# Kernel tuning notes

Hardware: AMD Instinct MI355X
Metric: run time of the kernel (lower is better)

The kernel has to match this reference:

```python
import jax, jax.numpy as jnp
import numpy as np

N, F_IN, HID, H1, E = 50000, 512, 128, 4, 800000
NEG_SLOPE = 0.2

def setup_inputs() -> dict:
    key = jax.random.key(0)
    ks = jax.random.split(key, 10)
    s = lambda fan: 1.0 / np.sqrt(fan)
    x = jax.random.normal(ks[0], (N, F_IN), jnp.float32)
    edge_index = jax.random.randint(ks[1], (2, E), 0, N, jnp.int32)
    W1 = jax.random.normal(ks[2], (F_IN, H1 * HID), jnp.float32) * s(F_IN)
    a_src1 = jax.random.normal(ks[3], (H1, HID), jnp.float32) * s(HID)
    a_dst1 = jax.random.normal(ks[4], (H1, HID), jnp.float32) * s(HID)
    b1 = jnp.zeros((H1 * HID,), jnp.float32)
    W2 = jax.random.normal(ks[5], (H1 * HID, HID), jnp.float32) * s(H1 * HID)
    a_src2 = jax.random.normal(ks[6], (1, HID), jnp.float32) * s(HID)
    a_dst2 = jax.random.normal(ks[7], (1, HID), jnp.float32) * s(HID)
    b2 = jnp.zeros((HID,), jnp.float32)
    return {"x": x, "edge_index": edge_index, "W1": W1, "a_src1": a_src1,
            "a_dst1": a_dst1, "b1": b1, "W2": W2, "a_src2": a_src2,
            "a_dst2": a_dst2, "b2": b2}

def _gat(x, src, dst, W, a_src, a_dst, b, n):
    H, C = a_src.shape
    h = (x @ W).reshape(-1, H, C)                      # [N, H, C]
    # per-edge attention logits: alpha_src[src] + alpha_dst[dst]
    e = jax.nn.leaky_relu((h * a_src).sum(-1)[src] + (h * a_dst).sum(-1)[dst],
                          NEG_SLOPE)                   # [E', H]
    # segment softmax over destination node
    m = jax.ops.segment_max(e, dst, num_segments=n)
    p = jnp.exp(e - m[dst])
    denom = jax.ops.segment_sum(p, dst, num_segments=n)
    alpha = p / (denom[dst] + 1e-16)
    # weighted scatter-add aggregation
    out = jax.ops.segment_sum(h[src] * alpha[:, :, None], dst, num_segments=n)
    return out.reshape(-1, H * C) + b

def reference(x, edge_index, W1, a_src1, a_dst1, b1, W2, a_src2, a_dst2, b2):
    loops = jnp.arange(N, dtype=edge_index.dtype)      # add_self_loops=True
    src = jnp.concatenate([edge_index[0], loops])
    dst = jnp.concatenate([edge_index[1], loops])
    h = jax.nn.elu(_gat(x, src, dst, W1, a_src1, a_dst1, b1, N))
    return _gat(h, src, dst, W2, a_src2, a_dst2, b2, N)
```

## Files before the change

### kernel.cpp

```cpp
#include <hip/hip_runtime.h>
#include <hip/hip_bf16.h>
#include <math.h>

#define NEG_SLOPE 0.2f

constexpr int N_NODES = 50000;
constexpr int F_IN    = 512;
constexpr int HID     = 128;
constexpr int H1      = 4;
constexpr int E_EDGES = 800000;
constexpr int E_TOT   = E_EDGES + N_NODES;

typedef __attribute__((ext_vector_type(8))) short short8;
typedef __attribute__((ext_vector_type(4))) float floatx4;
typedef __attribute__((ext_vector_type(4))) unsigned short ushort4v;

__device__ __forceinline__ unsigned short f2bf(float f) {
  union { float f; unsigned int u; } v; v.f = f;
  unsigned int u = v.u + 0x7FFFu + ((v.u >> 16) & 1u);
  return (unsigned short)(u >> 16);
}
__device__ __forceinline__ float bf_lo(unsigned int u) {
  union { unsigned int u; float f; } v; v.u = u << 16; return v.f;
}
__device__ __forceinline__ float bf_hi(unsigned int u) {
  union { unsigned int u; float f; } v; v.u = u & 0xFFFF0000u; return v.f;
}

__device__ __forceinline__ void store_val(float* p, float v) { *p = v; }
__device__ __forceinline__ void store_val(unsigned short* p, float v) { *p = f2bf(v); }

template <int CPT>
__device__ __forceinline__ void store_vec(unsigned short* p, const float* v) {
#pragma unroll
  for (int c = 0; c < CPT; c += 4) {
    ushort4v o;
#pragma unroll
    for (int j = 0; j < 4; ++j) o[j] = f2bf(v[c + j]);
    *(ushort4v*)(p + c) = o;
  }
}
template <int CPT>
__device__ __forceinline__ void store_vec(float* p, const float* v) {
#pragma unroll
  for (int c = 0; c < CPT; c += 4) *(float4*)(p + c) = *(const float4*)(v + c);
}

__device__ __forceinline__ void async_load16(const void* g, void* lds) {
  __builtin_amdgcn_global_load_lds(
      (const __attribute__((address_space(1))) unsigned int*)g,
      (__attribute__((address_space(3))) unsigned int*)lds, 16, 0, 0);
}

__global__ void zero_int_kernel(int* p, int n) {
  int i = blockIdx.x * blockDim.x + threadIdx.x;
  if (i < n) p[i] = 0;
}

__global__ void hist_kernel(const int* __restrict__ ei, int* __restrict__ counts) {
  int i = blockIdx.x * blockDim.x + threadIdx.x;
  if (i < E_EDGES) {
    atomicAdd(&counts[ei[E_EDGES + i]], 1);
  } else if (i < E_TOT) {
    atomicAdd(&counts[i - E_EDGES], 1);
  }
}

__global__ void scan1_kernel(const int* __restrict__ cnt, int* __restrict__ part,
                             int* __restrict__ bsum, int n) {
  __shared__ int buf[256];
  int tid = threadIdx.x, i = blockIdx.x * 256 + tid;
  int v = (i < n) ? cnt[i] : 0;
  buf[tid] = v;
  __syncthreads();
  for (int s = 1; s < 256; s <<= 1) {
    int t = (tid >= s) ? buf[tid - s] : 0;
    __syncthreads();
    buf[tid] += t;
    __syncthreads();
  }
  if (i < n) part[i] = buf[tid] - v;
  if (tid == 255) bsum[blockIdx.x] = buf[255];
}

__global__ void scan2_kernel(int* __restrict__ bsum, int nb) {
  __shared__ int buf[256];
  int tid = threadIdx.x;
  int v = (tid < nb) ? bsum[tid] : 0;
  buf[tid] = v;
  __syncthreads();
  for (int s = 1; s < 256; s <<= 1) {
    int t = (tid >= s) ? buf[tid - s] : 0;
    __syncthreads();
    buf[tid] += t;
    __syncthreads();
  }
  if (tid < nb) bsum[tid] = buf[tid] - v;
  if (tid == 255) bsum[nb] = buf[255];
}

__global__ void scan3_kernel(const int* __restrict__ part, const int* __restrict__ bsum,
                             int* __restrict__ offs, int* __restrict__ cursor, int n) {
  int i = blockIdx.x * 256 + threadIdx.x;
  if (i < n) { offs[i] = part[i] + bsum[blockIdx.x]; cursor[i] = 0; }
  if (i == 0) offs[n] = bsum[(n + 255) / 256];
}

__global__ void scatter_kernel(const int* __restrict__ ei, const int* __restrict__ offs,
                               int* __restrict__ cursor, int* __restrict__ sorted_src) {
  int i = blockIdx.x * blockDim.x + threadIdx.x;
  if (i >= E_TOT) return;
  int s, d;
  if (i < E_EDGES) { s = ei[i]; d = ei[E_EDGES + i]; }
  else             { s = i - E_EDGES; d = s; }
  int pos = offs[d] + atomicAdd(&cursor[d], 1);
  sorted_src[pos] = s;
}

__global__ void tcast_kernel(const float* __restrict__ in, unsigned short* __restrict__ out,
                             int K, int N) {
  int idx = blockIdx.x * blockDim.x + threadIdx.x;
  if (idx >= K * N) return;
  int n = idx / K, k = idx - n * K;
  out[idx] = f2bf(in[k * N + n]);
}

template <bool CVT_A, typename OT>
__global__ __launch_bounds__(256) void gemm_bf16_kernel(
    const void* __restrict__ Araw, const unsigned short* __restrict__ Bt,
    OT* __restrict__ C, const float* __restrict__ a_srcp, const float* __restrict__ a_dstp,
    float* __restrict__ alpha_src, float* __restrict__ alpha_dst,
    int M, int N, int K, int Hn, int nRowTiles) {
  __shared__ unsigned short As[128 * 32];
  __shared__ unsigned short Bs[128 * 32];
  __shared__ float red_s[128][2];
  __shared__ float red_d[128][2];

  int grp = blockIdx.x / (8 * Hn);
  int w8 = blockIdx.x % (8 * Hn);
  int head = w8 >> 3;
  int rowTile = grp * 8 + (w8 & 7);
  if (rowTile >= nRowTiles) return;
  int row0 = rowTile * 128;
  int col0 = head * 128;

  int tid = threadIdx.x;
  int lane = tid & 63, wave = tid >> 6;
  int wm = wave & 1, wn = wave >> 1;
  int l15 = lane & 15, quad = lane >> 4;

  floatx4 acc[4][4];
#pragma unroll
  for (int i = 0; i < 4; ++i)
#pragma unroll
    for (int j = 0; j < 4; ++j) acc[i][j] = (floatx4){0.f, 0.f, 0.f, 0.f};

  int seg_b = wave * 2;
  int r_in = (lane >> 2);
  int c8 = (lane & 3) * 8;

  for (int k0 = 0; k0 < K; k0 += 32) {
#pragma unroll
    for (int p = 0; p < 2; ++p) {
      int seg = seg_b + p;
      int r = seg * 16 + r_in;
      int gc = col0 + r;
      async_load16(Bt + (size_t)gc * K + k0 + c8, &Bs[seg * 512]);
    }
    if constexpr (CVT_A) {
      const float* Af = (const float*)Araw;
#pragma unroll
      for (int p = 0; p < 4; ++p) {
        int lin = tid + p * 256;
        int r = lin >> 3;
        int q = lin & 7;
        int gr = row0 + r; if (gr >= M) gr = M - 1;
        float4 f = *(const float4*)(Af + (size_t)gr * K + k0 + q * 4);
        ushort4v o;
        o[0] = f2bf(f.x); o[1] = f2bf(f.y); o[2] = f2bf(f.z); o[3] = f2bf(f.w);
        *(ushort4v*)&As[r * 32 + q * 4] = o;
      }
    } else {
      const unsigned short* Ab = (const unsigned short*)Araw;
#pragma unroll
      for (int p = 0; p < 2; ++p) {
        int seg = seg_b + p;
        int r = seg * 16 + r_in;
        int gr = row0 + r; if (gr >= M) gr = M - 1;
        async_load16(Ab + (size_t)gr * K + k0 + c8, &As[seg * 512]);
      }
    }
    __syncthreads();

    short8 a[4], b[4];
#pragma unroll
    for (int mi = 0; mi < 4; ++mi)
      a[mi] = *(const short8*)&As[(wm * 64 + mi * 16 + l15) * 32 + quad * 8];
#pragma unroll
    for (int ni = 0; ni < 4; ++ni)
      b[ni] = *(const short8*)&Bs[(wn * 64 + ni * 16 + l15) * 32 + quad * 8];
#pragma unroll
    for (int mi = 0; mi < 4; ++mi)
#pragma unroll
      for (int ni = 0; ni < 4; ++ni)
        acc[mi][ni] = __builtin_amdgcn_mfma_f32_16x16x32_bf16(a[mi], b[ni], acc[mi][ni], 0, 0, 0);
    __syncthreads();
  }

  float a_s[4], a_d[4];
#pragma unroll
  for (int ni = 0; ni < 4; ++ni) {
    int cih = wn * 64 + ni * 16 + l15;
    a_s[ni] = a_srcp[head * HID + cih];
    a_d[ni] = a_dstp[head * HID + cih];
  }

#pragma unroll
  for (int mi = 0; mi < 4; ++mi) {
#pragma unroll
    for (int r = 0; r < 4; ++r) {
      int rloc = wm * 64 + mi * 16 + quad * 4 + r;
      int grow = row0 + rloc;
      float ps = 0.f, pd = 0.f;
#pragma unroll
      for (int ni = 0; ni < 4; ++ni) {
        float v = acc[mi][ni][r];
        ps += v * a_s[ni];
        pd += v * a_d[ni];
        if (grow < M) {
          int gcol = col0 + wn * 64 + ni * 16 + l15;
          store_val(&C[(size_t)grow * N + gcol], v);
        }
      }
#pragma unroll
      for (int off = 1; off < 16; off <<= 1) {
        ps += __shfl_xor(ps, off);
        pd += __shfl_xor(pd, off);
      }
      if (l15 == 0) { red_s[rloc][wn] = ps; red_d[rloc][wn] = pd; }
    }
  }
  __syncthreads();
  if (tid < 128) {
    int grow = row0 + tid;
    if (grow < M) {
      alpha_src[(size_t)grow * Hn + head] = red_s[tid][0] + red_s[tid][1];
      alpha_dst[(size_t)grow * Hn + head] = red_d[tid][0] + red_d[tid][1];
    }
  }
}

template <int H, typename OT>
__global__ __launch_bounds__(64) void aggregate_kernel(
    const unsigned short* __restrict__ h, const float* __restrict__ asrc,
    const float* __restrict__ adst, const int* __restrict__ offs,
    const int* __restrict__ sorted_src, const float* __restrict__ bias,
    OT* __restrict__ out, int apply_elu) {
  constexpr int CPT = 8;
  constexpr int CH = H * HID;
  constexpr int NCH = CH / CPT;
  constexpr int SLOTS = 64 / NCH;
  __shared__ float p_sh[64 * H];
  __shared__ int rowoff_sh[64];
  int node = blockIdx.x;
  int lane = threadIdx.x;
  int off = offs[node];
  int deg = offs[node + 1] - off;
  if (deg > 64) deg = 64;

  int s_i = 0;
  if (lane < deg) s_i = sorted_src[off + lane];
  rowoff_sh[lane] = s_i * CH;

  float ar[H];
#pragma unroll
  for (int hh = 0; hh < H; ++hh) ar[hh] = (lane < deg) ? asrc[s_i * H + hh] : 0.f;
#pragma unroll
  for (int hh = 0; hh < H; ++hh) {
    float v = ar[hh] + adst[node * H + hh];
    v = (v > 0.f) ? v : NEG_SLOPE * v;
    float lg = (lane < deg) ? v : -1e30f;
#pragma unroll
    for (int o = 32; o; o >>= 1) lg = fmaxf(lg, __shfl_xor(lg, o));
    float p = (lane < deg) ? expf(v - lg) : 0.f;
    float s = p;
#pragma unroll
    for (int o = 32; o; o >>= 1) s += __shfl_xor(s, o);
    p_sh[lane * H + hh] = p * (1.f / (s + 1e-16f));
  }
  __syncthreads();

  int chlane = lane % NCH;
  int slot = lane / NCH;
  int ch = chlane * CPT;
  int head = ch >> 7;

  float acc[CPT];
#pragma unroll
  for (int c = 0; c < CPT; ++c) acc[c] = 0.f;

  auto body = [&](int e) {
    float w = p_sh[e * H + head];
    uint4 u = *(const uint4*)(h + (size_t)(unsigned)rowoff_sh[e] + ch);
    acc[0] += bf_lo(u.x) * w;  acc[1] += bf_hi(u.x) * w;
    acc[2] += bf_lo(u.y) * w;  acc[3] += bf_hi(u.y) * w;
    acc[4] += bf_lo(u.z) * w;  acc[5] += bf_hi(u.z) * w;
    acc[6] += bf_lo(u.w) * w;  acc[7] += bf_hi(u.w) * w;
  };
  int e = slot;
  for (; e + 7 * SLOTS < deg; e += 8 * SLOTS) {
    body(e); body(e + SLOTS); body(e + 2 * SLOTS); body(e + 3 * SLOTS);
    body(e + 4 * SLOTS); body(e + 5 * SLOTS); body(e + 6 * SLOTS); body(e + 7 * SLOTS);
  }
  for (; e + SLOTS < deg; e += 2 * SLOTS) { body(e); body(e + SLOTS); }
  for (; e < deg; e += SLOTS) body(e);

#pragma unroll
  for (int o = NCH; o < 64; o <<= 1)
#pragma unroll
    for (int c = 0; c < CPT; ++c) acc[c] += __shfl_xor(acc[c], o);

  if (slot == 0) {
    float r[CPT];
#pragma unroll
    for (int c = 0; c < CPT; ++c) {
      float t = acc[c] + bias[ch + c];
      if (apply_elu) t = (t > 0.f) ? t : (expf(t) - 1.f);
      r[c] = t;
    }
    store_vec<CPT>(&out[(size_t)node * CH + ch], r);
  }
}

extern "C" void kernel_launch(void* const* d_in, const int* in_sizes, int n_in,
                              void* d_out, int out_size, void* d_ws, size_t ws_size,
                              hipStream_t stream) {
  const float* x      = (const float*)d_in[0];
  const int*   ei     = (const int*)d_in[1];
  const float* W1     = (const float*)d_in[2];
  const float* a_src1 = (const float*)d_in[3];
  const float* a_dst1 = (const float*)d_in[4];
  const float* b1     = (const float*)d_in[5];
  const float* W2     = (const float*)d_in[6];
  const float* a_src2 = (const float*)d_in[7];
  const float* a_dst2 = (const float*)d_in[8];
  const float* b2     = (const float*)d_in[9];
  float* out = (float*)d_out;

  float* ws   = (float*)d_ws;
  float* as1  = ws;
  float* ad1  = as1 + N_NODES * H1;
  float* as2  = ad1 + N_NODES * H1;
  float* ad2  = as2 + N_NODES;
  unsigned short* bufA = (unsigned short*)(ad2 + N_NODES);
  unsigned short* bufB = bufA + (size_t)N_NODES * 512;
  unsigned short* hmidb = bufA;
  unsigned short* h1b   = bufB;
  unsigned short* h2b   = bufB;
  unsigned short* W1t   = bufB + (size_t)N_NODES * 512;
  unsigned short* W2t   = W1t + 512 * 512;
  int* counts = (int*)(W2t + 128 * 512);
  int* cursor = counts + N_NODES;
  int* offs   = cursor + N_NODES;
  int* ssrc   = offs + N_NODES + 1;
  int* part   = ssrc + E_TOT;
  int* bsum   = part + N_NODES;

  constexpr int NB = (N_NODES + 255) / 256;
  constexpr int NRT = (N_NODES + 127) / 128;
  constexpr int NRT8 = ((NRT + 7) / 8) * 8;

  zero_int_kernel<<<(N_NODES + 255) / 256, 256, 0, stream>>>(counts, N_NODES);
  hist_kernel<<<(E_TOT + 255) / 256, 256, 0, stream>>>(ei, counts);
  scan1_kernel<<<NB, 256, 0, stream>>>(counts, part, bsum, N_NODES);
  scan2_kernel<<<1, 256, 0, stream>>>(bsum, NB);
  scan3_kernel<<<NB, 256, 0, stream>>>(part, bsum, offs, cursor, N_NODES);
  scatter_kernel<<<(E_TOT + 255) / 256, 256, 0, stream>>>(ei, offs, cursor, ssrc);

  tcast_kernel<<<(512 * 512 + 255) / 256, 256, 0, stream>>>(W1, W1t, 512, 512);
  tcast_kernel<<<(512 * 128 + 255) / 256, 256, 0, stream>>>(W2, W2t, 512, 128);

  gemm_bf16_kernel<true, unsigned short><<<NRT8 * H1, 256, 0, stream>>>(
      x, W1t, h1b, a_src1, a_dst1, as1, ad1, N_NODES, 512, 512, H1, NRT);
  aggregate_kernel<4, unsigned short><<<N_NODES, 64, 0, stream>>>(
      h1b, as1, ad1, offs, ssrc, b1, hmidb, 1);

  gemm_bf16_kernel<false, unsigned short><<<NRT8, 256, 0, stream>>>(
      hmidb, W2t, h2b, a_src2, a_dst2, as2, ad2, N_NODES, 128, 512, 1, NRT);
  aggregate_kernel<1, float><<<N_NODES, 64, 0, stream>>>(
      h2b, as2, ad2, offs, ssrc, b2, out, 0);
}
```

Baseline: 508.5 us.

## Split aggregation across two waves per block for both GAT layers

```diff
diff --git a/kernel.cpp b/kernel.cpp
--- a/kernel.cpp
+++ b/kernel.cpp
@@ -250,34 +250,37 @@
   }
 }
 
-template <int H, typename OT>
-__global__ __launch_bounds__(64) void aggregate_kernel(
+template <int H, int WPN, typename OT>
+__global__ __launch_bounds__(128) void aggregate_kernel(
     const unsigned short* __restrict__ h, const float* __restrict__ asrc,
     const float* __restrict__ adst, const int* __restrict__ offs,
     const int* __restrict__ sorted_src, const float* __restrict__ bias,
     OT* __restrict__ out, int apply_elu) {
   constexpr int CPT = 8;
   constexpr int CH = H * HID;
-  constexpr int NCH = CH / CPT;
+  constexpr int WCH = CH / WPN;
+  constexpr int NCH = WCH / CPT;
   constexpr int SLOTS = 64 / NCH;
-  __shared__ float p_sh[64 * H];
-  __shared__ int rowoff_sh[64];
-  int node = blockIdx.x;
-  int lane = threadIdx.x;
-  int off = offs[node];
-  int deg = offs[node + 1] - off;
+  __shared__ float p_sh[2][64 * H];
+  __shared__ int ro_sh[2][64];
+  int tid = threadIdx.x;
+  int lane = tid & 63, w = tid >> 6;
+  int node = (WPN == 2) ? blockIdx.x : blockIdx.x * 2 + w;
+  bool live = node < N_NODES;
+  int off = live ? offs[node] : 0;
+  int deg = live ? (offs[node + 1] - off) : 0;
   if (deg > 64) deg = 64;
 
   int s_i = 0;
   if (lane < deg) s_i = sorted_src[off + lane];
-  rowoff_sh[lane] = s_i * CH;
+  ro_sh[w][lane] = s_i * CH;
 
   float ar[H];
 #pragma unroll
   for (int hh = 0; hh < H; ++hh) ar[hh] = (lane < deg) ? asrc[s_i * H + hh] : 0.f;
 #pragma unroll
   for (int hh = 0; hh < H; ++hh) {
-    float v = ar[hh] + adst[node * H + hh];
+    float v = ar[hh] + (live ? adst[node * H + hh] : 0.f);
     v = (v > 0.f) ? v : NEG_SLOPE * v;
     float lg = (lane < deg) ? v : -1e30f;
 #pragma unroll
@@ -286,26 +289,28 @@
     float s = p;
 #pragma unroll
     for (int o = 32; o; o >>= 1) s += __shfl_xor(s, o);
-    p_sh[lane * H + hh] = p * (1.f / (s + 1e-16f));
+    p_sh[w][lane * H + hh] = p * (1.f / (s + 1e-16f));
   }
   __syncthreads();
 
   int chlane = lane % NCH;
   int slot = lane / NCH;
-  int ch = chlane * CPT;
+  int ch = (WPN == 2 ? w * WCH : 0) + chlane * CPT;
   int head = ch >> 7;
 
   float acc[CPT];
 #pragma unroll
   for (int c = 0; c < CPT; ++c) acc[c] = 0.f;
 
+  const float* pw = &p_sh[w][0];
+  const int* ro = &ro_sh[w][0];
   auto body = [&](int e) {
-    float w = p_sh[e * H + head];
-    uint4 u = *(const uint4*)(h + (size_t)(unsigned)rowoff_sh[e] + ch);
-    acc[0] += bf_lo(u.x) * w;  acc[1] += bf_hi(u.x) * w;
-    acc[2] += bf_lo(u.y) * w;  acc[3] += bf_hi(u.y) * w;
-    acc[4] += bf_lo(u.z) * w;  acc[5] += bf_hi(u.z) * w;
-    acc[6] += bf_lo(u.w) * w;  acc[7] += bf_hi(u.w) * w;
+    float wt = pw[e * H + head];
+    uint4 u = *(const uint4*)(h + (size_t)(unsigned)ro[e] + ch);
+    acc[0] += bf_lo(u.x) * wt;  acc[1] += bf_hi(u.x) * wt;
+    acc[2] += bf_lo(u.y) * wt;  acc[3] += bf_hi(u.y) * wt;
+    acc[4] += bf_lo(u.z) * wt;  acc[5] += bf_hi(u.z) * wt;
+    acc[6] += bf_lo(u.w) * wt;  acc[7] += bf_hi(u.w) * wt;
   };
   int e = slot;
   for (; e + 7 * SLOTS < deg; e += 8 * SLOTS) {
@@ -320,7 +325,7 @@
 #pragma unroll
     for (int c = 0; c < CPT; ++c) acc[c] += __shfl_xor(acc[c], o);
 
-  if (slot == 0) {
+  if (live && slot == 0) {
     float r[CPT];
 #pragma unroll
     for (int c = 0; c < CPT; ++c) {
@@ -382,11 +387,11 @@
 
   gemm_bf16_kernel<true, unsigned short><<<NRT8 * H1, 256, 0, stream>>>(
       x, W1t, h1b, a_src1, a_dst1, as1, ad1, N_NODES, 512, 512, H1, NRT);
-  aggregate_kernel<4, unsigned short><<<N_NODES, 64, 0, stream>>>(
+  aggregate_kernel<4, 2, unsigned short><<<N_NODES, 128, 0, stream>>>(
       h1b, as1, ad1, offs, ssrc, b1, hmidb, 1);
 
   gemm_bf16_kernel<false, unsigned short><<<NRT8, 256, 0, stream>>>(
       hmidb, W2t, h2b, a_src2, a_dst2, as2, ad2, N_NODES, 128, 512, 1, NRT);
-  aggregate_kernel<1, float><<<N_NODES, 64, 0, stream>>>(
+  aggregate_kernel<1, 1, float><<<(N_NODES + 1) / 2, 128, 0, stream>>>(
       h2b, as2, ad2, offs, ssrc, b2, out, 0);
 }
```

After: 522.4 us. 2.7% more time.
